# Kernel tuning notes

Measured on AMD Instinct MI355X. Metric: run time of the kernel, lower is better.

Reference implementation:

```python
import jax, jax.numpy as jnp
import numpy as np

N = 50000
F_IN = 256
H1, D1 = 8, 8            # conv1: 8 heads x 8 dims, concat -> 64
H2, C = 8, 16            # conv2: 8 heads x num_classes, concat -> 128
NEG_SLOPE = 0.2


def setup_inputs() -> dict:
    key = jax.random.key(0)
    ks = jax.random.split(key, 10)
    x = jax.random.normal(ks[0], (N, F_IN), dtype=jnp.float32)
    edge_index = jax.random.randint(ks[1], (2, 800000), 0, N, dtype=jnp.int64)
    s1 = 1.0 / np.sqrt(F_IN)
    s2 = 1.0 / np.sqrt(H1 * D1)
    return {
        "x": x,
        "edge_index": edge_index,
        "W1": jax.random.normal(ks[2], (F_IN, H1 * D1), dtype=jnp.float32) * s1,
        "a1_src": jax.random.normal(ks[3], (H1, D1), dtype=jnp.float32) * s2,
        "a1_dst": jax.random.normal(ks[4], (H1, D1), dtype=jnp.float32) * s2,
        "b1": jnp.zeros((H1 * D1,), dtype=jnp.float32),
        "W2": jax.random.normal(ks[5], (H1 * D1, H2 * C), dtype=jnp.float32) * s2,
        "a2_src": jax.random.normal(ks[6], (H2, C), dtype=jnp.float32) * (1.0 / np.sqrt(C)),
        "a2_dst": jax.random.normal(ks[7], (H2, C), dtype=jnp.float32) * (1.0 / np.sqrt(C)),
        "b2": jnp.zeros((H2 * C,), dtype=jnp.float32),
    }


def _add_self_loops(edge_index, n):
    loops = jnp.arange(n, dtype=edge_index.dtype)
    return jnp.concatenate([edge_index, jnp.stack([loops, loops])], axis=1)


def _gat_conv(x, src, dst, W, a_src, a_dst, b, heads, out_dim, n):
    # xw: [N, H, O]
    xw = (x @ W).reshape(n, heads, out_dim)
    al_src = jnp.einsum("nho,ho->nh", xw, a_src)  # [N, H]
    al_dst = jnp.einsum("nho,ho->nh", xw, a_dst)
    e = jax.nn.leaky_relu(al_src[src] + al_dst[dst], NEG_SLOPE)  # [E, H]
    # segment softmax over edges sharing a destination node
    e_max = jax.ops.segment_max(e, dst, num_segments=n)
    e_exp = jnp.exp(e - e_max[dst])
    denom = jax.ops.segment_sum(e_exp, dst, num_segments=n)
    alpha = e_exp / (denom[dst] + 1e-16)                          # [E, H]
    msg = xw[src] * alpha[:, :, None]                              # [E, H, O]
    out = jax.ops.segment_sum(msg, dst, num_segments=n)           # [N, H, O]
    return out.reshape(n, heads * out_dim) + b, alpha


def reference(x, edge_index, W1, a1_src, a1_dst, b1, W2, a2_src, a2_dst, b2):
    ei = _add_self_loops(edge_index, N)
    src, dst = ei[0], ei[1]
    # dropout is a no-op at inference (training=False)
    h1, alpha1 = _gat_conv(x, src, dst, W1, a1_src, a1_dst, b1, H1, D1, N)
    h1 = jax.nn.elu(h1)
    h2, _ = _gat_conv(h1, src, dst, W2, a2_src, a2_dst, b2, H2, C, N)
    logp = jax.nn.log_softmax(h2, axis=1)
    return logp, alpha1
```

## Files before the change

### kernel.cpp

```cpp
#include <hip/hip_runtime.h>

#define N_NODES 50000
#define N_EDGES 800000
#define N_TOT   850000
#define NEG 0.2f
#define ELLW 64

#define G1_TILES 391
#define G2_TILES 782

__device__ __forceinline__ float leaky(float x) { return x > 0.f ? x : NEG * x; }

__device__ __forceinline__ unsigned bf16pk(float a, float b) {
  unsigned ua = __float_as_uint(a), ub = __float_as_uint(b);
  ua = (ua + 0x7FFFu + ((ua >> 16) & 1u)) >> 16;
  ub = (ub + 0x7FFFu + ((ub >> 16) & 1u)) >> 16;
  return ua | (ub << 16);
}
__device__ __forceinline__ float blo(unsigned u) { return __uint_as_float(u << 16); }
__device__ __forceinline__ float bhi(unsigned u) { return __uint_as_float(u & 0xFFFF0000u); }
__device__ __forceinline__ float bh2f(unsigned short h) { return __uint_as_float(((unsigned)h) << 16); }

__global__ __launch_bounds__(256) void gemm1_ell_k(const float* __restrict__ x,
    const float* __restrict__ W1, const float* __restrict__ a1sv, const float* __restrict__ a1dv,
    unsigned short* __restrict__ xw1h, float* __restrict__ al1s, float* __restrict__ a1dd,
    const int* __restrict__ srcA, const int* __restrict__ dstA,
    int* __restrict__ cnt, unsigned short* __restrict__ ell)
{
  __shared__ float xs[32 * 128];
  __shared__ float wsm[32 * 64];
  if (blockIdx.x >= G1_TILES) {
    int e = (blockIdx.x - G1_TILES) * 256 + threadIdx.x;
    if (e < N_EDGES) {
      int d = dstA[e], s = srcA[e];
      int p = atomicAdd(&cnt[d], 1);
      if (p < ELLW) ell[d * ELLW + p] = (unsigned short)s;
    }
    return;
  }
  const int t = threadIdx.x;
  const int tx = t & 15, ty = t >> 4;
  const int n0 = blockIdx.x * 128;
  const int nl = t >> 1;
  const int ks = (t & 1) * 16;
  const int wk = t >> 3;
  const int wc = (t & 7) * 8;
  int gn = n0 + nl; if (gn >= N_NODES) gn = N_NODES - 1;
  const float* xrowb = x + (size_t)gn * 256 + ks;

  float acc[8][4];
#pragma unroll
  for (int r = 0; r < 8; ++r)
#pragma unroll
    for (int i = 0; i < 4; ++i) acc[r][i] = 0.f;

  for (int kc = 0; kc < 8; ++kc) {
    const int kb = kc * 32;
    const float4* xp = (const float4*)(xrowb + kb);
    float4 v0 = xp[0], v1 = xp[1], v2 = xp[2], v3 = xp[3];
    const float* wrow = W1 + (size_t)(kb + wk) * 64 + wc;
    float4 w0 = ((const float4*)wrow)[0];
    float4 w1 = ((const float4*)wrow)[1];
    __syncthreads();
    xs[(ks + 0) * 128 + nl] = v0.x;  xs[(ks + 1) * 128 + nl] = v0.y;
    xs[(ks + 2) * 128 + nl] = v0.z;  xs[(ks + 3) * 128 + nl] = v0.w;
    xs[(ks + 4) * 128 + nl] = v1.x;  xs[(ks + 5) * 128 + nl] = v1.y;
    xs[(ks + 6) * 128 + nl] = v1.z;  xs[(ks + 7) * 128 + nl] = v1.w;
    xs[(ks + 8) * 128 + nl] = v2.x;  xs[(ks + 9) * 128 + nl] = v2.y;
    xs[(ks + 10) * 128 + nl] = v2.z; xs[(ks + 11) * 128 + nl] = v2.w;
    xs[(ks + 12) * 128 + nl] = v3.x; xs[(ks + 13) * 128 + nl] = v3.y;
    xs[(ks + 14) * 128 + nl] = v3.z; xs[(ks + 15) * 128 + nl] = v3.w;
    ((float4*)&wsm[wk * 64 + wc])[0] = w0;
    ((float4*)&wsm[wk * 64 + wc])[1] = w1;
    __syncthreads();
#pragma unroll 4
    for (int k = 0; k < 32; ++k) {
      float4 xa = *(const float4*)&xs[k * 128 + ty * 8];
      float4 xb = *(const float4*)&xs[k * 128 + ty * 8 + 4];
      float4 wv = *(const float4*)&wsm[k * 64 + tx * 4];
      float xn[8]; *(float4*)&xn[0] = xa; *(float4*)&xn[4] = xb;
      float wn[4]; *(float4*)wn = wv;
#pragma unroll
      for (int r = 0; r < 8; ++r)
#pragma unroll
        for (int i = 0; i < 4; ++i) acc[r][i] += xn[r] * wn[i];
    }
  }
  float cs[4], cd[4];
#pragma unroll
  for (int i = 0; i < 4; ++i) { cs[i] = a1sv[tx * 4 + i]; cd[i] = a1dv[tx * 4 + i]; }
#pragma unroll
  for (int r = 0; r < 8; ++r) {
    int n = n0 + ty * 8 + r;
    if (n >= N_NODES) break;
    uint2 pk;
    pk.x = bf16pk(acc[r][0], acc[r][1]);
    pk.y = bf16pk(acc[r][2], acc[r][3]);
    *(uint2*)(xw1h + (size_t)n * 64 + tx * 4) = pk;
    float ps = acc[r][0] * cs[0] + acc[r][1] * cs[1] + acc[r][2] * cs[2] + acc[r][3] * cs[3];
    float pd = acc[r][0] * cd[0] + acc[r][1] * cd[1] + acc[r][2] * cd[2] + acc[r][3] * cd[3];
    ps += __shfl_xor(ps, 1);
    pd += __shfl_xor(pd, 1);
    if ((tx & 1) == 0) {
      al1s[n * 8 + (tx >> 1)] = ps;
      a1dd[n * 16 + (tx >> 1)] = pd;
    }
  }
}

__global__ __launch_bounds__(256) void agg1_k(const unsigned short* __restrict__ xw1h,
    const float* __restrict__ al1s, float* __restrict__ a1dd,
    const int* __restrict__ cnt, const unsigned short* __restrict__ ell,
    const float* __restrict__ b1, float* __restrict__ h1)
{
  const int lane = threadIdx.x & 63;
  const int n = blockIdx.x * 4 + (threadIdx.x >> 6);
  if (n >= N_NODES) return;
  const int h = lane >> 3;
  const float ad = a1dd[n * 16 + h];
  float ws = __expf(leaky(al1s[n * 8 + h] + ad));
  float den0 = ws, den1r = 0.f;
  float acc0 = ws * bh2f(xw1h[(size_t)n * 64 + lane]), acc1 = 0.f;
  int num = cnt[n]; if (num > ELLW) num = ELLW;
  const uint4* cp = (const uint4*)(ell + (size_t)n * ELLW);
  int i = 0;
  for (; i + 8 <= num; i += 8) {
    uint4 A = cp[i >> 3];
    int s0 = A.x & 0xFFFF, s1 = (int)(A.x >> 16);
    int s2 = A.y & 0xFFFF, s3 = (int)(A.y >> 16);
    int s4 = A.z & 0xFFFF, s5 = (int)(A.z >> 16);
    int s6 = A.w & 0xFFFF, s7 = (int)(A.w >> 16);
    float l0 = al1s[s0 * 8 + h] + ad, l1 = al1s[s1 * 8 + h] + ad;
    float l2 = al1s[s2 * 8 + h] + ad, l3 = al1s[s3 * 8 + h] + ad;
    float l4 = al1s[s4 * 8 + h] + ad, l5 = al1s[s5 * 8 + h] + ad;
    float l6 = al1s[s6 * 8 + h] + ad, l7 = al1s[s7 * 8 + h] + ad;
    float v0 = bh2f(xw1h[(size_t)s0 * 64 + lane]), v1 = bh2f(xw1h[(size_t)s1 * 64 + lane]);
    float v2 = bh2f(xw1h[(size_t)s2 * 64 + lane]), v3 = bh2f(xw1h[(size_t)s3 * 64 + lane]);
    float v4 = bh2f(xw1h[(size_t)s4 * 64 + lane]), v5 = bh2f(xw1h[(size_t)s5 * 64 + lane]);
    float v6 = bh2f(xw1h[(size_t)s6 * 64 + lane]), v7 = bh2f(xw1h[(size_t)s7 * 64 + lane]);
    float w0 = __expf(leaky(l0)), w1 = __expf(leaky(l1));
    float w2 = __expf(leaky(l2)), w3 = __expf(leaky(l3));
    float w4 = __expf(leaky(l4)), w5 = __expf(leaky(l5));
    float w6 = __expf(leaky(l6)), w7 = __expf(leaky(l7));
    acc0 += w0 * v0; acc1 += w1 * v1; acc0 += w2 * v2; acc1 += w3 * v3;
    acc0 += w4 * v4; acc1 += w5 * v5; acc0 += w6 * v6; acc1 += w7 * v7;
    den0 += w0 + w2 + w4 + w6; den1r += w1 + w3 + w5 + w7;
  }
  for (; i + 4 <= num; i += 4) {
    uint2 A = *(const uint2*)(ell + (size_t)n * ELLW + i);
    int s0 = A.x & 0xFFFF, s1 = (int)(A.x >> 16);
    int s2 = A.y & 0xFFFF, s3 = (int)(A.y >> 16);
    float l0 = al1s[s0 * 8 + h] + ad, l1 = al1s[s1 * 8 + h] + ad;
    float l2 = al1s[s2 * 8 + h] + ad, l3 = al1s[s3 * 8 + h] + ad;
    float v0 = bh2f(xw1h[(size_t)s0 * 64 + lane]), v1 = bh2f(xw1h[(size_t)s1 * 64 + lane]);
    float v2 = bh2f(xw1h[(size_t)s2 * 64 + lane]), v3 = bh2f(xw1h[(size_t)s3 * 64 + lane]);
    float w0 = __expf(leaky(l0)), w1 = __expf(leaky(l1));
    float w2 = __expf(leaky(l2)), w3 = __expf(leaky(l3));
    acc0 += w0 * v0; acc1 += w1 * v1; acc0 += w2 * v2; acc1 += w3 * v3;
    den0 += w0 + w2; den1r += w1 + w3;
  }
  for (; i < num; ++i) {
    int s = ell[(size_t)n * ELLW + i];
    float w = __expf(leaky(al1s[s * 8 + h] + ad));
    acc0 += w * bh2f(xw1h[(size_t)s * 64 + lane]);
    den0 += w;
  }
  float den = den0 + den1r, acc = acc0 + acc1;
  if ((lane & 7) == 0) a1dd[n * 16 + 8 + h] = den;
  float o = acc / (den + 1e-16f) + b1[lane];
  h1[(size_t)n * 64 + lane] = o > 0.f ? o : (__expf(o) - 1.f);
}

__global__ __launch_bounds__(256) void gemm2_alpha_k(const float* __restrict__ h1,
    const float* __restrict__ W2, const float* __restrict__ a2sv, const float* __restrict__ a2dv,
    unsigned* __restrict__ xw2b, float* __restrict__ al2s, float* __restrict__ al2d,
    const int* __restrict__ srcA, const int* __restrict__ dstA,
    const float* __restrict__ al1s, const float* __restrict__ a1dd,
    float* __restrict__ alpha_out)
{
  __shared__ float xs[64 * 64];
  __shared__ float wsm[64 * 128];
  if (blockIdx.x >= G2_TILES) {
    int e = (blockIdx.x - G2_TILES) * 256 + threadIdx.x;
    if (e >= N_TOT) return;
    int s, d;
    if (e < N_EDGES) { s = srcA[e]; d = dstA[e]; }
    else             { s = d = e - N_EDGES; }
    float4 as0 = ((const float4*)(al1s + s * 8))[0];
    float4 as1 = ((const float4*)(al1s + s * 8))[1];
    const float4* dd = (const float4*)(a1dd + d * 16);
    float4 ad0 = dd[0];
    float4 ad1 = dd[1];
    float4 dn0 = dd[2];
    float4 dn1 = dd[3];
    float4 o0, o1;
    o0.x = __expf(leaky(as0.x + ad0.x)) / (dn0.x + 1e-16f);
    o0.y = __expf(leaky(as0.y + ad0.y)) / (dn0.y + 1e-16f);
    o0.z = __expf(leaky(as0.z + ad0.z)) / (dn0.z + 1e-16f);
    o0.w = __expf(leaky(as0.w + ad0.w)) / (dn0.w + 1e-16f);
    o1.x = __expf(leaky(as1.x + ad1.x)) / (dn1.x + 1e-16f);
    o1.y = __expf(leaky(as1.y + ad1.y)) / (dn1.y + 1e-16f);
    o1.z = __expf(leaky(as1.z + ad1.z)) / (dn1.z + 1e-16f);
    o1.w = __expf(leaky(as1.w + ad1.w)) / (dn1.w + 1e-16f);
    ((float4*)(alpha_out + (size_t)e * 8))[0] = o0;
    ((float4*)(alpha_out + (size_t)e * 8))[1] = o1;
    return;
  }
  const int t = threadIdx.x;
  const int tx = t & 15, ty = t >> 4;
  const int n0 = blockIdx.x * 64;
  {
    const int nl = t >> 2;
    const int ks = (t & 3) * 16;
    int gn = n0 + nl; if (gn >= N_NODES) gn = N_NODES - 1;
    const float4* hp = (const float4*)(h1 + (size_t)gn * 64 + ks);
#pragma unroll
    for (int j = 0; j < 4; ++j) {
      float4 v = hp[j];
      xs[(ks + 4 * j + 0) * 64 + nl] = v.x;
      xs[(ks + 4 * j + 1) * 64 + nl] = v.y;
      xs[(ks + 4 * j + 2) * 64 + nl] = v.z;
      xs[(ks + 4 * j + 3) * 64 + nl] = v.w;
    }
    const int wk = t >> 2;
    const int wc = (t & 3) * 32;
    const float4* wp = (const float4*)(W2 + (size_t)wk * 128 + wc);
    float4* wd = (float4*)&wsm[wk * 128 + wc];
#pragma unroll
    for (int j = 0; j < 8; ++j) wd[j] = wp[j];
  }
  __syncthreads();
  float acc[4][8];
#pragma unroll
  for (int r = 0; r < 4; ++r)
#pragma unroll
    for (int i = 0; i < 8; ++i) acc[r][i] = 0.f;
#pragma unroll 4
  for (int k = 0; k < 64; ++k) {
    float4 xa = *(const float4*)&xs[k * 64 + ty * 4];
    float4 wa = *(const float4*)&wsm[k * 128 + tx * 8];
    float4 wb = *(const float4*)&wsm[k * 128 + tx * 8 + 4];
    float xn[4]; *(float4*)xn = xa;
    float wn[8]; *(float4*)&wn[0] = wa; *(float4*)&wn[4] = wb;
#pragma unroll
    for (int r = 0; r < 4; ++r)
#pragma unroll
      for (int i = 0; i < 8; ++i) acc[r][i] += xn[r] * wn[i];
  }
  float cs[8], cd[8];
#pragma unroll
  for (int i = 0; i < 8; ++i) { cs[i] = a2sv[tx * 8 + i]; cd[i] = a2dv[tx * 8 + i]; }
#pragma unroll
  for (int r = 0; r < 4; ++r) {
    int n = n0 + ty * 4 + r;
    if (n >= N_NODES) break;
    uint4 pk;
    pk.x = bf16pk(acc[r][0], acc[r][1]);
    pk.y = bf16pk(acc[r][2], acc[r][3]);
    pk.z = bf16pk(acc[r][4], acc[r][5]);
    pk.w = bf16pk(acc[r][6], acc[r][7]);
    *(uint4*)(xw2b + (size_t)n * 64 + tx * 4) = pk;
    float ps = 0.f, pd = 0.f;
#pragma unroll
    for (int i = 0; i < 8; ++i) { ps += acc[r][i] * cs[i]; pd += acc[r][i] * cd[i]; }
    ps += __shfl_xor(ps, 1);
    pd += __shfl_xor(pd, 1);
    if ((tx & 1) == 0) {
      al2s[n * 8 + (tx >> 1)] = ps;
      al2d[n * 8 + (tx >> 1)] = pd;
    }
  }
}

__global__ __launch_bounds__(256) void agg2_k(const unsigned* __restrict__ xw2b,
    const float* __restrict__ al2s, const float* __restrict__ al2d,
    const int* __restrict__ cnt, const unsigned short* __restrict__ ell,
    const float* __restrict__ b2, float* __restrict__ logp)
{
  const int lane = threadIdx.x & 63;
  const int n = blockIdx.x * 4 + (threadIdx.x >> 6);
  if (n >= N_NODES) return;
  const int h = lane >> 3;
  const float ad = al2d[n * 8 + h];
  float ws = __expf(leaky(al2s[n * 8 + h] + ad));
  unsigned su = xw2b[(size_t)n * 64 + lane];
  float den0 = ws, den1r = 0.f;
  float ax0 = ws * blo(su), ay0 = ws * bhi(su), ax1 = 0.f, ay1 = 0.f;
  int num = cnt[n]; if (num > ELLW) num = ELLW;
  const uint4* cp = (const uint4*)(ell + (size_t)n * ELLW);
  int i = 0;
  for (; i + 8 <= num; i += 8) {
    uint4 A = cp[i >> 3];
    int s0 = A.x & 0xFFFF, s1 = (int)(A.x >> 16);
    int s2 = A.y & 0xFFFF, s3 = (int)(A.y >> 16);
    int s4 = A.z & 0xFFFF, s5 = (int)(A.z >> 16);
    int s6 = A.w & 0xFFFF, s7 = (int)(A.w >> 16);
    float l0 = al2s[s0 * 8 + h] + ad, l1 = al2s[s1 * 8 + h] + ad;
    float l2 = al2s[s2 * 8 + h] + ad, l3 = al2s[s3 * 8 + h] + ad;
    float l4 = al2s[s4 * 8 + h] + ad, l5 = al2s[s5 * 8 + h] + ad;
    float l6 = al2s[s6 * 8 + h] + ad, l7 = al2s[s7 * 8 + h] + ad;
    unsigned u0 = xw2b[(size_t)s0 * 64 + lane], u1 = xw2b[(size_t)s1 * 64 + lane];
    unsigned u2 = xw2b[(size_t)s2 * 64 + lane], u3 = xw2b[(size_t)s3 * 64 + lane];
    unsigned u4 = xw2b[(size_t)s4 * 64 + lane], u5 = xw2b[(size_t)s5 * 64 + lane];
    unsigned u6 = xw2b[(size_t)s6 * 64 + lane], u7 = xw2b[(size_t)s7 * 64 + lane];
    float w0 = __expf(leaky(l0)), w1 = __expf(leaky(l1));
    float w2 = __expf(leaky(l2)), w3 = __expf(leaky(l3));
    float w4 = __expf(leaky(l4)), w5 = __expf(leaky(l5));
    float w6 = __expf(leaky(l6)), w7 = __expf(leaky(l7));
    ax0 += w0 * blo(u0); ay0 += w0 * bhi(u0);
    ax1 += w1 * blo(u1); ay1 += w1 * bhi(u1);
    ax0 += w2 * blo(u2); ay0 += w2 * bhi(u2);
    ax1 += w3 * blo(u3); ay1 += w3 * bhi(u3);
    ax0 += w4 * blo(u4); ay0 += w4 * bhi(u4);
    ax1 += w5 * blo(u5); ay1 += w5 * bhi(u5);
    ax0 += w6 * blo(u6); ay0 += w6 * bhi(u6);
    ax1 += w7 * blo(u7); ay1 += w7 * bhi(u7);
    den0 += w0 + w2 + w4 + w6; den1r += w1 + w3 + w5 + w7;
  }
  for (; i + 4 <= num; i += 4) {
    uint2 A = *(const uint2*)(ell + (size_t)n * ELLW + i);
    int s0 = A.x & 0xFFFF, s1 = (int)(A.x >> 16);
    int s2 = A.y & 0xFFFF, s3 = (int)(A.y >> 16);
    float l0 = al2s[s0 * 8 + h] + ad, l1 = al2s[s1 * 8 + h] + ad;
    float l2 = al2s[s2 * 8 + h] + ad, l3 = al2s[s3 * 8 + h] + ad;
    unsigned u0 = xw2b[(size_t)s0 * 64 + lane], u1 = xw2b[(size_t)s1 * 64 + lane];
    unsigned u2 = xw2b[(size_t)s2 * 64 + lane], u3 = xw2b[(size_t)s3 * 64 + lane];
    float w0 = __expf(leaky(l0)), w1 = __expf(leaky(l1));
    float w2 = __expf(leaky(l2)), w3 = __expf(leaky(l3));
    ax0 += w0 * blo(u0); ay0 += w0 * bhi(u0);
    ax1 += w1 * blo(u1); ay1 += w1 * bhi(u1);
    ax0 += w2 * blo(u2); ay0 += w2 * bhi(u2);
    ax1 += w3 * blo(u3); ay1 += w3 * bhi(u3);
    den0 += w0 + w2; den1r += w1 + w3;
  }
  for (; i < num; ++i) {
    int s = ell[(size_t)n * ELLW + i];
    float w = __expf(leaky(al2s[s * 8 + h] + ad));
    unsigned u = xw2b[(size_t)s * 64 + lane];
    ax0 += w * blo(u); ay0 += w * bhi(u); den0 += w;
  }
  float inv = 1.f / (den0 + den1r + 1e-16f);
  float o0 = (ax0 + ax1) * inv + b2[2 * lane];
  float o1 = (ay0 + ay1) * inv + b2[2 * lane + 1];
  float mx = fmaxf(o0, o1);
#pragma unroll
  for (int off = 1; off < 64; off <<= 1) mx = fmaxf(mx, __shfl_xor(mx, off));
  float se = __expf(o0 - mx) + __expf(o1 - mx);
#pragma unroll
  for (int off = 1; off < 64; off <<= 1) se += __shfl_xor(se, off);
  float lse = mx + __logf(se);
  float2 o; o.x = o0 - lse; o.y = o1 - lse;
  ((float2*)logp)[(size_t)n * 64 + lane] = o;
}

extern "C" void kernel_launch(void* const* d_in, const int* in_sizes, int n_in,
                              void* d_out, int out_size, void* d_ws, size_t ws_size,
                              hipStream_t stream)
{
  const float* x   = (const float*)d_in[0];
  const int*   ei  = (const int*)d_in[1];
  const float* W1  = (const float*)d_in[2];
  const float* a1s = (const float*)d_in[3];
  const float* a1d = (const float*)d_in[4];
  const float* b1  = (const float*)d_in[5];
  const float* W2  = (const float*)d_in[6];
  const float* a2s = (const float*)d_in[7];
  const float* a2d = (const float*)d_in[8];
  const float* b2  = (const float*)d_in[9];
  const int* srcA = ei;
  const int* dstA = ei + N_EDGES;

  char* ws = (char*)d_ws;
  unsigned short* xw1h = (unsigned short*)ws;            ws += (size_t)N_NODES * 64 * 2;
  float* h1    = (float*)ws;  ws += (size_t)N_NODES * 64 * 4;
  unsigned* xw2b = (unsigned*)ws; ws += (size_t)N_NODES * 64 * 4;
  float* al1s_ = (float*)ws;  ws += (size_t)N_NODES * 8 * 4;
  float* a1dd_ = (float*)ws;  ws += (size_t)N_NODES * 16 * 4;
  float* al2s_ = (float*)ws;  ws += (size_t)N_NODES * 8 * 4;
  float* al2d_ = (float*)ws;  ws += (size_t)N_NODES * 8 * 4;
  int* cnt    = (int*)ws;     ws += (size_t)N_NODES * 4;
  unsigned short* ell = (unsigned short*)ws; ws += (size_t)N_NODES * ELLW * 2;

  float* logp      = (float*)d_out;
  float* alpha_out = logp + (size_t)N_NODES * 128;

  hipMemsetAsync(cnt, 0, N_NODES * sizeof(int), stream);

  gemm1_ell_k<<<G1_TILES + (N_EDGES + 255) / 256, 256, 0, stream>>>(
      x, W1, a1s, a1d, xw1h, al1s_, a1dd_, srcA, dstA, cnt, ell);
  agg1_k<<<(N_NODES + 3) / 4, 256, 0, stream>>>(xw1h, al1s_, a1dd_, cnt, ell, b1, h1);
  gemm2_alpha_k<<<G2_TILES + (N_TOT + 255) / 256, 256, 0, stream>>>(
      h1, W2, a2s, a2d, xw2b, al2s_, al2d_, srcA, dstA, al1s_, a1dd_, alpha_out);
  agg2_k<<<(N_NODES + 3) / 4, 256, 0, stream>>>(xw2b, al2s_, al2d_, cnt, ell, b2, logp);
}
```

Before: 164.4 us.

## Pre-bin edges by destination range before ELL scatter and align aggregation blocks

Adds a binning pass that groups edges into 8 destination-node ranges through shared-memory buffers, then has the ELL scatter blocks read one bin each. The aim is to keep the atomic counter and ELL writes for a block within one node range, so they hit cache instead of scattering across all nodes. The aggregation kernels now map block IDs so that interleaved blocks cover each bin's node range, which changes the order in which nodes are scheduled. The cost is an extra kernel launch plus a write and read of a packed bin buffer.

```diff
diff --git a/kernel.cpp b/kernel.cpp
--- a/kernel.cpp
+++ b/kernel.cpp
@@ -9,6 +9,14 @@
 #define G1_TILES 391
 #define G2_TILES 782
 
+#define NPB   6250
+#define BINB  131072
+#define EPB   4096
+#define BINCAP 736
+#define NBINBLK 196
+#define NSCAT 448
+#define AGG_SUB 1563
+
 __device__ __forceinline__ float leaky(float x) { return x > 0.f ? x : NEG * x; }
 
 __device__ __forceinline__ unsigned bf16pk(float a, float b) {
@@ -21,18 +29,63 @@
 __device__ __forceinline__ float bhi(unsigned u) { return __uint_as_float(u & 0xFFFF0000u); }
 __device__ __forceinline__ float bh2f(unsigned short h) { return __uint_as_float(((unsigned)h) << 16); }
 
+__global__ __launch_bounds__(256) void bin_k(const int* __restrict__ srcA,
+    const int* __restrict__ dstA, unsigned* __restrict__ bins, int* __restrict__ bcnt)
+{
+  __shared__ unsigned buf[8][BINCAP];
+  __shared__ int bc[8], bbase[8];
+  const int t = threadIdx.x;
+  if (t < 8) bc[t] = 0;
+  __syncthreads();
+  const int i40 = blockIdx.x * (EPB / 4);
+#pragma unroll
+  for (int j = 0; j < 4; ++j) {
+    int i4 = i40 + j * 256 + t;
+    if (i4 < N_EDGES / 4) {
+      int4 s4 = ((const int4*)srcA)[i4];
+      int4 d4 = ((const int4*)dstA)[i4];
+      int dd[4] = {d4.x, d4.y, d4.z, d4.w};
+      int ss[4] = {s4.x, s4.y, s4.z, s4.w};
+#pragma unroll
+      for (int q = 0; q < 4; ++q) {
+        int bin = dd[q] / NPB;
+        unsigned rec = (unsigned)dd[q] | ((unsigned)ss[q] << 16);
+        int p = atomicAdd(&bc[bin], 1);
+        if (p < BINCAP) buf[bin][p] = rec;
+        else { int g = atomicAdd(&bcnt[bin], 1); bins[bin * BINB + g] = rec; }
+      }
+    }
+  }
+  __syncthreads();
+  if (t < 8) {
+    int c = bc[t]; if (c > BINCAP) c = BINCAP;
+    bbase[t] = atomicAdd(&bcnt[t], c);
+    bc[t] = c;
+  }
+  __syncthreads();
+  for (int b = 0; b < 8; ++b) {
+    int c = bc[b], base = bbase[b];
+    for (int i = t; i < c; i += 256)
+      bins[b * BINB + base + i] = buf[b][i];
+  }
+}
+
 __global__ __launch_bounds__(256) void gemm1_ell_k(const float* __restrict__ x,
     const float* __restrict__ W1, const float* __restrict__ a1sv, const float* __restrict__ a1dv,
     unsigned short* __restrict__ xw1h, float* __restrict__ al1s, float* __restrict__ a1dd,
-    const int* __restrict__ srcA, const int* __restrict__ dstA,
+    const unsigned* __restrict__ bins, const int* __restrict__ bcnt,
     int* __restrict__ cnt, unsigned short* __restrict__ ell)
 {
   __shared__ float xs[32 * 128];
   __shared__ float wsm[32 * 64];
-  if (blockIdx.x >= G1_TILES) {
-    int e = (blockIdx.x - G1_TILES) * 256 + threadIdx.x;
-    if (e < N_EDGES) {
-      int d = dstA[e], s = srcA[e];
+  if (blockIdx.x < NSCAT) {
+    const int bin = blockIdx.x & 7;
+    const int sub = blockIdx.x >> 3;
+    const int m = bcnt[bin];
+    const unsigned* bp = bins + (size_t)bin * BINB;
+    for (int i = sub * 256 + threadIdx.x; i < m; i += (NSCAT / 8) * 256) {
+      unsigned rec = bp[i];
+      int d = rec & 0xFFFFu, s = rec >> 16;
       int p = atomicAdd(&cnt[d], 1);
       if (p < ELLW) ell[d * ELLW + p] = (unsigned short)s;
     }
@@ -40,7 +93,7 @@
   }
   const int t = threadIdx.x;
   const int tx = t & 15, ty = t >> 4;
-  const int n0 = blockIdx.x * 128;
+  const int n0 = (blockIdx.x - NSCAT) * 128;
   const int nl = t >> 1;
   const int ks = (t & 1) * 16;
   const int wk = t >> 3;
@@ -114,8 +167,10 @@
     const float* __restrict__ b1, float* __restrict__ h1)
 {
   const int lane = threadIdx.x & 63;
-  const int n = blockIdx.x * 4 + (threadIdx.x >> 6);
-  if (n >= N_NODES) return;
+  const int bin = blockIdx.x & 7, sub = blockIdx.x >> 3;
+  const int local = sub * 4 + (threadIdx.x >> 6);
+  if (local >= NPB) return;
+  const int n = bin * NPB + local;
   const int h = lane >> 3;
   const float ad = a1dd[n * 16 + h];
   float ws = __expf(leaky(al1s[n * 8 + h] + ad));
@@ -278,8 +333,10 @@
     const float* __restrict__ b2, float* __restrict__ logp)
 {
   const int lane = threadIdx.x & 63;
-  const int n = blockIdx.x * 4 + (threadIdx.x >> 6);
-  if (n >= N_NODES) return;
+  const int bin = blockIdx.x & 7, sub = blockIdx.x >> 3;
+  const int local = sub * 4 + (threadIdx.x >> 6);
+  if (local >= NPB) return;
+  const int n = bin * NPB + local;
   const int h = lane >> 3;
   const float ad = al2d[n * 8 + h];
   float ws = __expf(leaky(al2s[n * 8 + h] + ad));
@@ -379,17 +436,20 @@
   float* al2s_ = (float*)ws;  ws += (size_t)N_NODES * 8 * 4;
   float* al2d_ = (float*)ws;  ws += (size_t)N_NODES * 8 * 4;
   int* cnt    = (int*)ws;     ws += (size_t)N_NODES * 4;
+  int* bcnt   = (int*)ws;     ws += 8 * 4;
   unsigned short* ell = (unsigned short*)ws; ws += (size_t)N_NODES * ELLW * 2;
+  unsigned* bins = (unsigned*)ws; ws += (size_t)8 * BINB * 4;
 
   float* logp      = (float*)d_out;
   float* alpha_out = logp + (size_t)N_NODES * 128;
 
-  hipMemsetAsync(cnt, 0, N_NODES * sizeof(int), stream);
-
-  gemm1_ell_k<<<G1_TILES + (N_EDGES + 255) / 256, 256, 0, stream>>>(
-      x, W1, a1s, a1d, xw1h, al1s_, a1dd_, srcA, dstA, cnt, ell);
-  agg1_k<<<(N_NODES + 3) / 4, 256, 0, stream>>>(xw1h, al1s_, a1dd_, cnt, ell, b1, h1);
+  hipMemsetAsync(cnt, 0, N_NODES * sizeof(int) + 8 * sizeof(int), stream);
+
+  bin_k<<<NBINBLK, 256, 0, stream>>>(srcA, dstA, bins, bcnt);
+  gemm1_ell_k<<<NSCAT + G1_TILES, 256, 0, stream>>>(
+      x, W1, a1s, a1d, xw1h, al1s_, a1dd_, bins, bcnt, cnt, ell);
+  agg1_k<<<8 * AGG_SUB, 256, 0, stream>>>(xw1h, al1s_, a1dd_, cnt, ell, b1, h1);
   gemm2_alpha_k<<<G2_TILES + (N_TOT + 255) / 256, 256, 0, stream>>>(
       h1, W2, a2s, a2d, xw2b, al2s_, al2d_, srcA, dstA, al1s_, a1dd_, alpha_out);
-  agg2_k<<<(N_NODES + 3) / 4, 256, 0, stream>>>(xw2b, al2s_, al2d_, cnt, ell, b2, logp);
-}
+  agg2_k<<<8 * AGG_SUB, 256, 0, stream>>>(xw2b, al2s_, al2d_, cnt, ell, b2, logp);
+}
```

Result: slower. 175.0 us (+6.4%).

## Build ELL adjacency via two-pass LDS binning instead of global atomics

Applied to the files above, without the earlier changes.

Replaces the per-edge global atomicAdd scatter into the ELL adjacency with two passes. A new kernel bins edges by destination range into per-block slot buffers in shared memory, with a small overflow list. Then blocks inside gemm1 build each 200-node ELL slice in LDS and write it out coalesced. This is meant to cut global atomic contention and scattered 2-byte writes, at the cost of an extra launch, extra workspace traffic, and every ELL block scanning the overflow list.

```diff
diff --git a/kernel.cpp b/kernel.cpp
--- a/kernel.cpp
+++ b/kernel.cpp
@@ -9,6 +9,14 @@
 #define G1_TILES 391
 #define G2_TILES 782
 
+#define NBIN   250
+#define NPBIN  200
+#define BKBLK  200
+#define EPBK   4000
+#define BCAP   40
+#define OCAP   4096
+#define NELLB  250
+
 __device__ __forceinline__ float leaky(float x) { return x > 0.f ? x : NEG * x; }
 
 __device__ __forceinline__ unsigned bf16pk(float a, float b) {
@@ -21,26 +29,89 @@
 __device__ __forceinline__ float bhi(unsigned u) { return __uint_as_float(u & 0xFFFF0000u); }
 __device__ __forceinline__ float bh2f(unsigned short h) { return __uint_as_float(((unsigned)h) << 16); }
 
+__global__ __launch_bounds__(256) void bin_k(const int* __restrict__ srcA,
+    const int* __restrict__ dstA, unsigned* __restrict__ slots,
+    unsigned short* __restrict__ bcnt2, unsigned* __restrict__ ofl, int* __restrict__ ofc)
+{
+  __shared__ unsigned buf[NBIN][BCAP];
+  __shared__ int bc[NBIN];
+  const int t = threadIdx.x;
+  for (int k = t; k < NBIN; k += 256) bc[k] = 0;
+  __syncthreads();
+  const int e0 = blockIdx.x * EPBK;
+#pragma unroll
+  for (int j = 0; j < 4; ++j) {
+    int i4 = j * 256 + t;
+    if (i4 < EPBK / 4) {
+      int4 s4 = ((const int4*)(srcA + e0))[i4];
+      int4 d4 = ((const int4*)(dstA + e0))[i4];
+      int dd[4] = {d4.x, d4.y, d4.z, d4.w};
+      int ss[4] = {s4.x, s4.y, s4.z, s4.w};
+#pragma unroll
+      for (int q = 0; q < 4; ++q) {
+        int bin = dd[q] / NPBIN;
+        unsigned rec = (unsigned)dd[q] | ((unsigned)ss[q] << 16);
+        int p = atomicAdd(&bc[bin], 1);
+        if (p < BCAP) buf[bin][p] = rec;
+        else { int g = atomicAdd(ofc, 1); if (g < OCAP) ofl[g] = rec; }
+      }
+    }
+  }
+  __syncthreads();
+  if (t < NBIN) {
+    int c = bc[t]; if (c > BCAP) c = BCAP;
+    bcnt2[(size_t)t * BKBLK + blockIdx.x] = (unsigned short)c;
+    unsigned* dp = slots + ((size_t)t * BKBLK + blockIdx.x) * BCAP;
+    for (int j = 0; j < c; ++j) dp[j] = buf[t][j];
+  }
+}
+
 __global__ __launch_bounds__(256) void gemm1_ell_k(const float* __restrict__ x,
     const float* __restrict__ W1, const float* __restrict__ a1sv, const float* __restrict__ a1dv,
     unsigned short* __restrict__ xw1h, float* __restrict__ al1s, float* __restrict__ a1dd,
-    const int* __restrict__ srcA, const int* __restrict__ dstA,
+    const unsigned* __restrict__ slots, const unsigned short* __restrict__ bcnt2,
+    const unsigned* __restrict__ ofl, const int* __restrict__ ofc,
     int* __restrict__ cnt, unsigned short* __restrict__ ell)
 {
-  __shared__ float xs[32 * 128];
-  __shared__ float wsm[32 * 64];
-  if (blockIdx.x >= G1_TILES) {
-    int e = (blockIdx.x - G1_TILES) * 256 + threadIdx.x;
-    if (e < N_EDGES) {
-      int d = dstA[e], s = srcA[e];
-      int p = atomicAdd(&cnt[d], 1);
-      if (p < ELLW) ell[d * ELLW + p] = (unsigned short)s;
-    }
+  __shared__ __align__(16) char smem[26432];
+  const int t = threadIdx.x;
+  if (blockIdx.x < NELLB) {
+    unsigned short* ell_lds = (unsigned short*)smem;
+    int* cnt_lds = (int*)(smem + 25600);
+    const int b = blockIdx.x;
+    for (int k = t; k < NPBIN; k += 256) cnt_lds[k] = 0;
+    __syncthreads();
+    if (t < BKBLK) {
+      int c = bcnt2[(size_t)b * BKBLK + t];
+      const unsigned* sp = slots + ((size_t)b * BKBLK + t) * BCAP;
+      for (int j = 0; j < c; ++j) {
+        unsigned rec = sp[j];
+        int row = (int)(rec & 0xFFFFu) - b * NPBIN;
+        int p = atomicAdd(&cnt_lds[row], 1);
+        if (p < ELLW) ell_lds[row * ELLW + p] = (unsigned short)(rec >> 16);
+      }
+    }
+    __syncthreads();
+    int oc = *ofc; if (oc > OCAP) oc = OCAP;
+    for (int i = t; i < oc; i += 256) {
+      unsigned rec = ofl[i];
+      int d = rec & 0xFFFFu;
+      if (d >= b * NPBIN && d < (b + 1) * NPBIN) {
+        int p = atomicAdd(&cnt_lds[d - b * NPBIN], 1);
+        if (p < ELLW) ell_lds[(d - b * NPBIN) * ELLW + p] = (unsigned short)(rec >> 16);
+      }
+    }
+    __syncthreads();
+    const uint4* s4 = (const uint4*)ell_lds;
+    uint4* d4 = (uint4*)(ell + (size_t)b * NPBIN * ELLW);
+    for (int i = t; i < NPBIN * ELLW / 8; i += 256) d4[i] = s4[i];
+    for (int k = t; k < NPBIN; k += 256) cnt[b * NPBIN + k] = cnt_lds[k];
     return;
   }
-  const int t = threadIdx.x;
+  float* xs  = (float*)smem;
+  float* wsm = (float*)(smem + 16384);
   const int tx = t & 15, ty = t >> 4;
-  const int n0 = blockIdx.x * 128;
+  const int n0 = (blockIdx.x - NELLB) * 128;
   const int nl = t >> 1;
   const int ks = (t & 1) * 16;
   const int wk = t >> 3;
@@ -380,14 +451,19 @@
   float* al2d_ = (float*)ws;  ws += (size_t)N_NODES * 8 * 4;
   int* cnt    = (int*)ws;     ws += (size_t)N_NODES * 4;
   unsigned short* ell = (unsigned short*)ws; ws += (size_t)N_NODES * ELLW * 2;
+  unsigned* slots = (unsigned*)ws; ws += (size_t)NBIN * BKBLK * BCAP * 4;
+  unsigned short* bcnt2 = (unsigned short*)ws; ws += (size_t)NBIN * BKBLK * 2;
+  unsigned* ofl = (unsigned*)ws; ws += (size_t)OCAP * 4;
+  int* ofc = (int*)ws; ws += 16;
 
   float* logp      = (float*)d_out;
   float* alpha_out = logp + (size_t)N_NODES * 128;
 
-  hipMemsetAsync(cnt, 0, N_NODES * sizeof(int), stream);
-
-  gemm1_ell_k<<<G1_TILES + (N_EDGES + 255) / 256, 256, 0, stream>>>(
-      x, W1, a1s, a1d, xw1h, al1s_, a1dd_, srcA, dstA, cnt, ell);
+  hipMemsetAsync(ofc, 0, sizeof(int), stream);
+
+  bin_k<<<BKBLK, 256, 0, stream>>>(srcA, dstA, slots, bcnt2, ofl, ofc);
+  gemm1_ell_k<<<NELLB + G1_TILES, 256, 0, stream>>>(
+      x, W1, a1s, a1d, xw1h, al1s_, a1dd_, slots, bcnt2, ofl, ofc, cnt, ell);
   agg1_k<<<(N_NODES + 3) / 4, 256, 0, stream>>>(xw1h, al1s_, a1dd_, cnt, ell, b1, h1);
   gemm2_alpha_k<<<G2_TILES + (N_TOT + 255) / 256, 256, 0, stream>>>(
       h1, W2, a2s, a2d, xw2b, al2s_, al2d_, srcA, dstA, al1s_, a1dd_, alpha_out);
```

Result: faster. 160.6 us (-2.3%).
